# Kernel tuning notes

Measured on AMD Instinct MI355X. Metric: run time of the kernel, lower is better.

## Reference

```python
import jax, jax.numpy as jnp
import numpy as np

H = 8          # num_heads
KD = 64        # key_dim
R = 256        # num_random_features
EPS = 1e-3     # kernel_epsilon
SCALE = 1.0 / np.sqrt(KD)
CHUNK = 128    # chunk size for causal scan (math identical to full cumsum)


def setup_inputs() -> dict:
    key = jax.random.key(0)
    ks = jax.random.split(key, 7)
    B, S, D = 4, 4096, H * KD
    x = jax.random.normal(ks[0], (B, S, D), dtype=jnp.float32)
    Wq = jax.random.normal(ks[1], (D, D), dtype=jnp.float32) * 0.02
    Wk = jax.random.normal(ks[2], (D, D), dtype=jnp.float32) * 0.02
    Wv = jax.random.normal(ks[3], (D, D), dtype=jnp.float32) * 0.02
    Wo = jax.random.normal(ks[4], (D, D), dtype=jnp.float32) * 0.02
    bo = jnp.zeros((D,), dtype=jnp.float32)
    # random_features: orthogonal rows within each KD block (keras 'orthogonal' init approx)
    g = jax.random.normal(ks[5], (R, KD), dtype=jnp.float32)
    rf = jnp.concatenate([jnp.linalg.qr(b.T)[0].T for b in g.reshape(R // KD, KD, KD)], axis=0)
    return {"x": x, "Wq": Wq, "Wk": Wk, "Wv": Wv, "Wo": Wo, "bo": bo, "rf": rf}


def _kernel_features(z, rf):
    # z: [B,S,H,KD] -> [B,S,H,R]; scale applied AFTER projection as in source
    p = jnp.einsum('bshd,rd->bshr', z, rf) * SCALE
    p = p - jnp.max(p, axis=-1, keepdims=True)
    return jnp.exp(p) + EPS


def _causal_favor(qf, kf, v):
    # qf,kf: [B,S,H,R]; v: [B,S,H,KD]. Equivalent to cumsum of bshrd outer products.
    B, S, _, _ = qf.shape
    nc = S // CHUNK
    def to_chunks(t):
        return jnp.moveaxis(t.reshape(B, nc, CHUNK, *t.shape[2:]), 1, 0)
    qc_all, kc_all, vc_all = to_chunks(qf), to_chunks(kf), to_chunks(v)

    @jax.checkpoint
    def step(carry, inp):
        S0, Z0 = carry                     # S0: [B,H,R,KD], Z0: [B,H,R]
        qc, kc, vc = inp                   # [B,C,H,R], [B,C,H,R], [B,C,H,KD]
        kv = jnp.einsum('bchr,bchd->bchrd', kc, vc)
        kv_cum = jnp.cumsum(kv, axis=1) + S0[:, None]
        num = jnp.einsum('bchr,bchrd->bchd', qc, kv_cum)
        z_cum = jnp.cumsum(kc, axis=1) + Z0[:, None]
        den = jnp.einsum('bchr,bchr->bch', qc, z_cum) + EPS
        out = num / den[..., None]
        return (kv_cum[:, -1], z_cum[:, -1]), out

    S0 = jnp.zeros((B, H, R, KD), dtype=qf.dtype)
    Z0 = jnp.zeros((B, H, R), dtype=qf.dtype)
    _, outs = jax.lax.scan(step, (S0, Z0), (qc_all, kc_all, vc_all))
    return jnp.moveaxis(outs, 0, 1).reshape(B, S, H, KD)


def reference(x, Wq, Wk, Wv, Wo, bo, rf):
    B, S, D = x.shape
    q = (x @ Wq).reshape(B, S, H, KD)
    k = (x @ Wk).reshape(B, S, H, KD)
    v = (x @ Wv).reshape(B, S, H, KD)
    qf = _kernel_features(q, rf)
    kf = _kernel_features(k, rf)
    attn = _causal_favor(qf, kf, v)        # [B,S,H,KD]
    attn = attn.reshape(B, S, H * KD)
    return attn @ Wo + bo
```

## Files before the change

### kernel.cpp

```cpp
#include <hip/hip_runtime.h>
#include <stdint.h>


namespace {
constexpr int kB = 4;
constexpr int kS = 4096;
constexpr int kH = 8;
constexpr int kD = 512;
constexpr int kR = 256;
constexpr int kNC = 32;
constexpr float kEPS = 1e-3f;
constexpr float kSCALE = 0.125f;
constexpr int kSP = 80;
constexpr int kSST = kSP * 256;
}

typedef __attribute__((ext_vector_type(8))) short bf16x8;
typedef __attribute__((ext_vector_type(4))) float f32x4;

__device__ __forceinline__ f32x4 mfma16(bf16x8 a, bf16x8 b, f32x4 c) {
  return __builtin_amdgcn_mfma_f32_16x16x32_bf16(a, b, c, 0, 0, 0);
}

__device__ __forceinline__ float bflo(uint32_t w) {
  union { uint32_t u; float f; } c; c.u = w << 16; return c.f;
}
__device__ __forceinline__ float bfhi(uint32_t w) {
  union { uint32_t u; float f; } c; c.u = w & 0xffff0000u; return c.f;
}
__device__ __forceinline__ uint16_t f2bf(float x) {
  union { float f; uint32_t i; } c; c.f = x;
  uint32_t r = c.i + 0x7fffu + ((c.i >> 16) & 1u);
  return (uint16_t)(r >> 16);
}

__global__ __launch_bounds__(256) void cast_inputs(
    const float* __restrict__ x, const float* __restrict__ rfm,
    uint16_t* __restrict__ x16, uint16_t* __restrict__ rf16)
{
  int i4 = blockIdx.x * 256 + threadIdx.x;
  const int n1 = 2097152;
  const int n2 = 4096;
  const float* src; uint16_t* dst; int off;
  if (i4 < n1) { src = x; dst = x16; off = i4; }
  else if (i4 < n1 + n2) { src = rfm; dst = rf16; off = i4 - n1; }
  else return;
  float4 v = *(const float4*)(src + (size_t)off * 4);
  uint2 o;
  o.x = (uint32_t)f2bf(v.x) | ((uint32_t)f2bf(v.y) << 16);
  o.y = (uint32_t)f2bf(v.z) | ((uint32_t)f2bf(v.w) << 16);
  *(uint2*)(dst + (size_t)off * 4) = o;
}

__global__ __launch_bounds__(256) void transpose_w(
    const float* __restrict__ Wq, const float* __restrict__ Wk,
    const float* __restrict__ Wv, const float* __restrict__ Wo,
    uint16_t* __restrict__ WtBase)
{
  __shared__ uint16_t t16[64][72];
  const int z = blockIdx.z;
  const float* W = (z == 0) ? Wq : (z == 1) ? Wk : (z == 2) ? Wv : Wo;
  uint16_t* Wt = WtBase + (size_t)z * 262144;
  const int tid = threadIdx.x;
  const int k0 = blockIdx.x * 64, n0 = blockIdx.y * 64;
#pragma unroll
  for (int i = 0; i < 4; ++i) {
    int idx = tid + 256 * i;
    int kk = idx >> 4, nn4 = (idx & 15) * 4;
    float4 v = *(const float4*)(W + (size_t)(k0 + kk) * 512 + n0 + nn4);
    t16[kk][nn4 + 0] = f2bf(v.x);
    t16[kk][nn4 + 1] = f2bf(v.y);
    t16[kk][nn4 + 2] = f2bf(v.z);
    t16[kk][nn4 + 3] = f2bf(v.w);
  }
  __syncthreads();
#pragma unroll
  for (int i = 0; i < 4; ++i) {
    int idx = tid + 256 * i;
    int nn = idx >> 4, kk4 = (idx & 15) * 4;
    uint2 o;
    o.x = (uint32_t)t16[kk4 + 0][nn] | ((uint32_t)t16[kk4 + 1][nn] << 16);
    o.y = (uint32_t)t16[kk4 + 2][nn] | ((uint32_t)t16[kk4 + 3][nn] << 16);
    *(uint2*)(Wt + (size_t)(n0 + nn) * 512 + k0 + kk4) = o;
  }
}

template <bool BF16OUT>
__global__ __launch_bounds__(256) void gemm_bf16(
    const uint16_t* __restrict__ A, const uint16_t* __restrict__ Bt,
    const float* __restrict__ bias, void* __restrict__ O)
{
  const int tid = threadIdx.x;
  const int w = tid >> 6, lane = tid & 63;
  const int lr = lane & 15, lg = lane >> 4;
  const int m_base = blockIdx.x * 128 + w * 32;
  const int n_base = blockIdx.y * 64;

  f32x4 acc[2][4];
#pragma unroll
  for (int mf = 0; mf < 2; ++mf)
#pragma unroll
    for (int nf = 0; nf < 4; ++nf) acc[mf][nf] = (f32x4){0.f, 0.f, 0.f, 0.f};

  const uint16_t* a0p = A + (size_t)(m_base + lr) * 512 + 8 * lg;
  const uint16_t* a1p = a0p + (size_t)16 * 512;
  const uint16_t* bp = Bt + (size_t)(n_base + lr) * 512 + 8 * lg;

#pragma unroll
  for (int ks = 0; ks < 16; ++ks) {
    bf16x8 a0 = *(const bf16x8*)(a0p + ks * 32);
    bf16x8 a1 = *(const bf16x8*)(a1p + ks * 32);
#pragma unroll
    for (int nf = 0; nf < 4; ++nf) {
      bf16x8 b = *(const bf16x8*)(bp + (size_t)nf * 16 * 512 + ks * 32);
      acc[0][nf] = mfma16(a0, b, acc[0][nf]);
      acc[1][nf] = mfma16(a1, b, acc[1][nf]);
    }
  }

  float badd[4];
#pragma unroll
  for (int nf = 0; nf < 4; ++nf)
    badd[nf] = bias ? bias[n_base + nf * 16 + lr] : 0.0f;

  if constexpr (BF16OUT) {
    __shared__ uint16_t tr[4][32][72];
#pragma unroll
    for (int mf = 0; mf < 2; ++mf)
#pragma unroll
      for (int nf = 0; nf < 4; ++nf)
#pragma unroll
        for (int reg = 0; reg < 4; ++reg)
          tr[w][mf * 16 + 4 * lg + reg][nf * 16 + lr] = f2bf(acc[mf][nf][reg] + badd[nf]);
    __syncthreads();
#pragma unroll
    for (int it = 0; it < 4; ++it) {
      int idx = it * 64 + lane;
      int row = idx >> 3, c8 = (idx & 7) * 8;
      uint4 val = *(const uint4*)&tr[w][row][c8];
      *(uint4*)((uint16_t*)O + (size_t)(m_base + row) * 512 + n_base + c8) = val;
    }
  } else {
    __shared__ float trf[4][32][68];
#pragma unroll
    for (int mf = 0; mf < 2; ++mf)
#pragma unroll
      for (int nf = 0; nf < 4; ++nf)
#pragma unroll
        for (int reg = 0; reg < 4; ++reg)
          trf[w][mf * 16 + 4 * lg + reg][nf * 16 + lr] = acc[mf][nf][reg] + badd[nf];
    __syncthreads();
#pragma unroll
    for (int it = 0; it < 8; ++it) {
      int idx = it * 64 + lane;
      int row = idx >> 4, c4 = (idx & 15) * 4;
      float4 val = *(const float4*)&trf[w][row][c4];
      *(float4*)((float*)O + (size_t)(m_base + row) * 512 + n_base + c4) = val;
    }
  }
}

__global__ __launch_bounds__(256) void feat_mfma(
    const uint16_t* __restrict__ q16, const uint16_t* __restrict__ k16,
    const uint16_t* __restrict__ rf16,
    uint16_t* __restrict__ qf, uint16_t* __restrict__ kf)
{
  __shared__ uint16_t tr[4][16][264];
  const uint16_t* src = blockIdx.y ? k16 : q16;
  uint16_t* dst = blockIdx.y ? kf : qf;
  const int tgrp = blockIdx.x >> 3, h = blockIdx.x & 7;
  const int tid = threadIdx.x;
  const int w = tid >> 6, lane = tid & 63;
  const int lr = lane & 15, lg = lane >> 4;
  const int t0 = tgrp * 64 + w * 16;

  f32x4 acc[16];
#pragma unroll
  for (int nf = 0; nf < 16; ++nf) acc[nf] = (f32x4){0.f, 0.f, 0.f, 0.f};

  const uint16_t* ap = src + (size_t)(t0 + lr) * 512 + h * 64 + 8 * lg;
#pragma unroll
  for (int ks = 0; ks < 2; ++ks) {
    bf16x8 a = *(const bf16x8*)(ap + ks * 32);
#pragma unroll
    for (int nf = 0; nf < 16; ++nf) {
      bf16x8 b = *(const bf16x8*)(rf16 + (size_t)(nf * 16 + lr) * 64 + ks * 32 + 8 * lg);
      acc[nf] = mfma16(a, b, acc[nf]);
    }
  }

  float mx[4] = {-1e30f, -1e30f, -1e30f, -1e30f};
#pragma unroll
  for (int nf = 0; nf < 16; ++nf)
#pragma unroll
    for (int reg = 0; reg < 4; ++reg) {
      acc[nf][reg] *= kSCALE;
      mx[reg] = fmaxf(mx[reg], acc[nf][reg]);
    }
#pragma unroll
  for (int reg = 0; reg < 4; ++reg) {
    mx[reg] = fmaxf(mx[reg], __shfl_xor(mx[reg], 1));
    mx[reg] = fmaxf(mx[reg], __shfl_xor(mx[reg], 2));
    mx[reg] = fmaxf(mx[reg], __shfl_xor(mx[reg], 4));
    mx[reg] = fmaxf(mx[reg], __shfl_xor(mx[reg], 8));
  }
#pragma unroll
  for (int nf = 0; nf < 16; ++nf)
#pragma unroll
    for (int reg = 0; reg < 4; ++reg)
      tr[w][4 * lg + reg][nf * 16 + lr] = f2bf(__expf(acc[nf][reg] - mx[reg]) + kEPS);
  __syncthreads();
#pragma unroll
  for (int it = 0; it < 8; ++it) {
    int idx = it * 64 + lane;
    int row = idx >> 5, c8 = (idx & 31) * 8;
    uint4 val = *(const uint4*)&tr[w][row][c8];
    *(uint4*)(dst + ((size_t)(t0 + row) * 8 + h) * 256 + c8) = val;
  }
}

__global__ __launch_bounds__(256) void chunk_mfma(
    const uint16_t* __restrict__ kfeat, const uint16_t* __restrict__ vbuf,
    uint16_t* __restrict__ Skv)
{
  __shared__ uint16_t Vaug[80][136];
  __shared__ uint16_t uni2[21120];
  uint16_t (*kfT)[72] = (uint16_t (*)[72])uni2;
  uint16_t (*outT)[264] = (uint16_t (*)[264])uni2;

  const int c = blockIdx.x, bh = blockIdx.y;
  const int b = bh >> 3, h = bh & 7;
  const int tid = threadIdx.x;
  const int w = tid >> 6, lane = tid & 63;
  const int lr = lane & 15, lg = lane >> 4;
  const size_t srow = (size_t)b * kS + (size_t)c * 128;

#pragma unroll
  for (int i = 0; i < 4; ++i) {
    int idx = tid + 256 * i;
    int u = idx & 127, d = (idx >> 7) * 8;
    uint4 w8 = *(const uint4*)(vbuf + (srow + u) * kD + h * 64 + d);
    Vaug[d + 0][u] = (uint16_t)(w8.x & 0xffff);
    Vaug[d + 1][u] = (uint16_t)(w8.x >> 16);
    Vaug[d + 2][u] = (uint16_t)(w8.y & 0xffff);
    Vaug[d + 3][u] = (uint16_t)(w8.y >> 16);
    Vaug[d + 4][u] = (uint16_t)(w8.z & 0xffff);
    Vaug[d + 5][u] = (uint16_t)(w8.z >> 16);
    Vaug[d + 6][u] = (uint16_t)(w8.w & 0xffff);
    Vaug[d + 7][u] = (uint16_t)(w8.w >> 16);
  }
  if (tid < 128) Vaug[64][tid] = 0x3F80;
  if (tid < 136) {
#pragma unroll
    for (int rr = 65; rr < 80; ++rr) Vaug[rr][tid] = 0;
  }

  f32x4 acc[5][4];
#pragma unroll
  for (int mf = 0; mf < 5; ++mf)
#pragma unroll
    for (int nf = 0; nf < 4; ++nf) acc[mf][nf] = (f32x4){0.f, 0.f, 0.f, 0.f};

  const uint16_t* kp0 = kfeat + (srow * kH + h) * kR;
#pragma unroll
  for (int th = 0; th < 2; ++th) {
    if (th) __syncthreads();
    const uint16_t* kp = kp0 + (size_t)th * 64 * (kH * kR);
#pragma unroll
    for (int i = 0; i < 16; ++i) {
      int idx = tid + 256 * i;
      int t = idx >> 6, c4 = idx & 63;
      uint2 wv = *(const uint2*)(kp + (size_t)t * (kH * kR) + c4 * 4);
      int r = c4 * 4;
      kfT[r + 0][t] = (uint16_t)(wv.x & 0xffff);
      kfT[r + 1][t] = (uint16_t)(wv.x >> 16);
      kfT[r + 2][t] = (uint16_t)(wv.y & 0xffff);
      kfT[r + 3][t] = (uint16_t)(wv.y >> 16);
    }
    __syncthreads();
#pragma unroll
    for (int ks = 0; ks < 2; ++ks) {
      bf16x8 af[5];
#pragma unroll
      for (int mf = 0; mf < 5; ++mf)
        af[mf] = *(const bf16x8*)&Vaug[mf * 16 + lr][th * 64 + ks * 32 + 8 * lg];
#pragma unroll
      for (int nf = 0; nf < 4; ++nf) {
        bf16x8 kb = *(const bf16x8*)&kfT[w * 64 + nf * 16 + lr][ks * 32 + 8 * lg];
#pragma unroll
        for (int mf = 0; mf < 5; ++mf)
          acc[mf][nf] = mfma16(af[mf], kb, acc[mf][nf]);
      }
    }
  }

  __syncthreads();
#pragma unroll
  for (int mf = 0; mf < 5; ++mf)
#pragma unroll
    for (int nf = 0; nf < 4; ++nf)
#pragma unroll
      for (int reg = 0; reg < 4; ++reg)
        outT[mf * 16 + 4 * lg + reg][w * 64 + nf * 16 + lr] = f2bf(acc[mf][nf][reg]);
  __syncthreads();

  uint16_t* So = Skv + ((size_t)bh * kNC + c) * kSST;
#pragma unroll
  for (int it = 0; it < 10; ++it) {
    int idx = tid + 256 * it;
    int row = idx >> 5, c8 = (idx & 31) * 8;
    uint4 val = *(const uint4*)&outT[row][c8];
    *(uint4*)(So + (size_t)row * 256 + c8) = val;
  }
}

__global__ __launch_bounds__(256) void prefix_kernel(uint16_t* __restrict__ Skv)
{
  int e = blockIdx.x * 256 + threadIdx.x;
  int bh = e / kSST;
  int rd = e - bh * kSST;
  size_t base = (size_t)bh * kNC * kSST + rd;
  float run = 0.f;
  for (int c = 0; c < kNC; ++c) {
    size_t idx = base + (size_t)c * kSST;
    union { uint32_t i; float f; } cv; cv.i = ((uint32_t)Skv[idx]) << 16;
    Skv[idx] = f2bf(run);
    run += cv.f;
  }
}

__global__ __launch_bounds__(256) void favor_mfma(
    const uint16_t* __restrict__ qfeat, const uint16_t* __restrict__ kfeat,
    const uint16_t* __restrict__ vbuf, const uint16_t* __restrict__ Skv,
    uint16_t* __restrict__ attn16)
{
  __shared__ uint16_t Vaug[80][136];
  __shared__ uint16_t A_l[4][32][40];

  const int c = blockIdx.x, bh = blockIdx.y;
  const int b = bh >> 3, h = bh & 7;
  const int tid = threadIdx.x;
  const int w = tid >> 6, lane = tid & 63;
  const int lr = lane & 15, lg = lane >> 4;
  const size_t srow = (size_t)b * kS + (size_t)c * 128;

#pragma unroll
  for (int i = 0; i < 4; ++i) {
    int idx = tid + 256 * i;
    int u = idx & 127, d = (idx >> 7) * 8;
    uint4 w8 = *(const uint4*)(vbuf + (srow + u) * kD + h * 64 + d);
    Vaug[d + 0][u] = (uint16_t)(w8.x & 0xffff);
    Vaug[d + 1][u] = (uint16_t)(w8.x >> 16);
    Vaug[d + 2][u] = (uint16_t)(w8.y & 0xffff);
    Vaug[d + 3][u] = (uint16_t)(w8.y >> 16);
    Vaug[d + 4][u] = (uint16_t)(w8.z & 0xffff);
    Vaug[d + 5][u] = (uint16_t)(w8.z >> 16);
    Vaug[d + 6][u] = (uint16_t)(w8.w & 0xffff);
    Vaug[d + 7][u] = (uint16_t)(w8.w >> 16);
  }
  if (tid < 128) Vaug[64][tid] = 0x3F80;
  if (tid < 136) {
#pragma unroll
    for (int rr = 65; rr < 80; ++rr) Vaug[rr][tid] = 0;
  }

  bf16x8 qa[2][8];
  const uint16_t* qp = qfeat + ((srow + w * 32 + lr) * kH + h) * kR + 8 * lg;
#pragma unroll
  for (int mf = 0; mf < 2; ++mf)
#pragma unroll
    for (int ks = 0; ks < 8; ++ks)
      qa[mf][ks] = *(const bf16x8*)(qp + (size_t)mf * 16 * (kH * kR) + ks * 32);

  f32x4 o[2][5];
#pragma unroll
  for (int mf = 0; mf < 2; ++mf)
#pragma unroll
    for (int nf = 0; nf < 5; ++nf) o[mf][nf] = (f32x4){0.f, 0.f, 0.f, 0.f};

  const uint16_t* Sg = Skv + ((size_t)bh * kNC + c) * kSST + 8 * lg;
#pragma unroll
  for (int ks = 0; ks < 8; ++ks) {
#pragma unroll
    for (int nf = 0; nf < 5; ++nf) {
      bf16x8 sb = *(const bf16x8*)(Sg + (size_t)(nf * 16 + lr) * 256 + ks * 32);
      o[0][nf] = mfma16(qa[0][ks], sb, o[0][nf]);
      o[1][nf] = mfma16(qa[1][ks], sb, o[1][nf]);
    }
  }

  __syncthreads();

  const uint16_t* kp = kfeat + (srow + lr) * (kH * kR) + h * kR + 8 * lg;
  for (int ut = 0; ut <= w; ++ut) {
    f32x4 aacc[2][2];
#pragma unroll
    for (int mf = 0; mf < 2; ++mf)
#pragma unroll
      for (int nf = 0; nf < 2; ++nf) aacc[mf][nf] = (f32x4){0.f, 0.f, 0.f, 0.f};
#pragma unroll
    for (int ks = 0; ks < 8; ++ks) {
      bf16x8 kb0 = *(const bf16x8*)(kp + (size_t)(ut * 32) * (kH * kR) + ks * 32);
      bf16x8 kb1 = *(const bf16x8*)(kp + (size_t)(ut * 32 + 16) * (kH * kR) + ks * 32);
      aacc[0][0] = mfma16(qa[0][ks], kb0, aacc[0][0]);
      aacc[0][1] = mfma16(qa[0][ks], kb1, aacc[0][1]);
      aacc[1][0] = mfma16(qa[1][ks], kb0, aacc[1][0]);
      aacc[1][1] = mfma16(qa[1][ks], kb1, aacc[1][1]);
    }
#pragma unroll
    for (int mf = 0; mf < 2; ++mf)
#pragma unroll
      for (int nf = 0; nf < 2; ++nf)
#pragma unroll
        for (int reg = 0; reg < 4; ++reg) {
          int trow = mf * 16 + 4 * lg + reg;
          int ucol = nf * 16 + lr;
          float v = aacc[mf][nf][reg];
          if (ut == w && ucol > trow) v = 0.0f;
          A_l[w][trow][ucol] = f2bf(v);
        }
    bf16x8 af0 = *(const bf16x8*)&A_l[w][lr][8 * lg];
    bf16x8 af1 = *(const bf16x8*)&A_l[w][16 + lr][8 * lg];
#pragma unroll
    for (int nf = 0; nf < 5; ++nf) {
      bf16x8 vb = *(const bf16x8*)&Vaug[nf * 16 + lr][ut * 32 + 8 * lg];
      o[0][nf] = mfma16(af0, vb, o[0][nf]);
      o[1][nf] = mfma16(af1, vb, o[1][nf]);
    }
  }

#pragma unroll
  for (int mf = 0; mf < 2; ++mf) {
    float inv[4];
#pragma unroll
    for (int reg = 0; reg < 4; ++reg) {
      float den = __shfl(o[mf][4][reg], lane & 48);
      inv[reg] = 1.0f / (den + kEPS);
    }
    const size_t trow = srow + w * 32 + mf * 16 + 4 * lg;
#pragma unroll
    for (int reg = 0; reg < 4; ++reg) {
      uint16_t* op = attn16 + (trow + reg) * kD + h * 64 + lr;
#pragma unroll
      for (int nf = 0; nf < 4; ++nf)
        op[nf * 16] = f2bf(o[mf][nf][reg] * inv[reg]);
    }
  }
}

extern "C" void kernel_launch(void* const* d_in, const int* in_sizes, int n_in,
                              void* d_out, int out_size, void* d_ws, size_t ws_size,
                              hipStream_t stream)
{
  (void)in_sizes; (void)n_in; (void)out_size; (void)ws_size;
  const float* x  = (const float*)d_in[0];
  const float* Wq = (const float*)d_in[1];
  const float* Wk = (const float*)d_in[2];
  const float* Wv = (const float*)d_in[3];
  const float* Wo = (const float*)d_in[4];
  const float* bo = (const float*)d_in[5];
  const float* rf = (const float*)d_in[6];
  float* out = (float*)d_out;

  char* ws = (char*)d_ws;
  uint16_t* x16   = (uint16_t*)ws;
  uint16_t* k16   = (uint16_t*)(ws + (16u << 20));
  uint16_t* v16   = (uint16_t*)(ws + (32u << 20));
  uint16_t* qf    = (uint16_t*)(ws + (48u << 20));
  uint16_t* kf    = (uint16_t*)(ws + (112u << 20));
  uint16_t* Skv   = (uint16_t*)(ws + (176u << 20));
  uint16_t* Wt    = (uint16_t*)(ws + (216u << 20));
  uint16_t* rf16  = Wt + 4 * 262144;
  uint16_t* q16   = (uint16_t*)d_out;
  uint16_t* attn16 = k16;

  cast_inputs<<<dim3(8208, 1, 1), 256, 0, stream>>>(x, rf, x16, rf16);
  transpose_w<<<dim3(8, 8, 4), 256, 0, stream>>>(Wq, Wk, Wv, Wo, Wt);

  gemm_bf16<true><<<dim3(128, 8, 1), 256, 0, stream>>>(x16, Wt + 0 * 262144, nullptr, q16);
  gemm_bf16<true><<<dim3(128, 8, 1), 256, 0, stream>>>(x16, Wt + 1 * 262144, nullptr, k16);
  gemm_bf16<true><<<dim3(128, 8, 1), 256, 0, stream>>>(x16, Wt + 2 * 262144, nullptr, v16);

  feat_mfma<<<dim3(2048, 2, 1), 256, 0, stream>>>(q16, k16, rf16, qf, kf);

  chunk_mfma<<<dim3(kNC, kB * kH, 1), 256, 0, stream>>>(kf, v16, Skv);
  prefix_kernel<<<dim3(2560, 1, 1), 256, 0, stream>>>(Skv);
  favor_mfma<<<dim3(kNC, kB * kH, 1), 256, 0, stream>>>(qf, kf, v16, Skv, attn16);

  gemm_bf16<false><<<dim3(128, 8, 1), 256, 0, stream>>>(attn16, Wt + 3 * 262144, bo, out);
}
```

Baseline: 397.2 us.

## Fold random-feature projection into Wq/Wk and fuse QK projection with feature map

```diff
diff --git a/kernel.cpp b/kernel.cpp
--- a/kernel.cpp
+++ b/kernel.cpp
@@ -36,15 +36,19 @@
 
 __global__ __launch_bounds__(256) void cast_inputs(
     const float* __restrict__ x, const float* __restrict__ rfm,
-    uint16_t* __restrict__ x16, uint16_t* __restrict__ rf16)
+    const float* __restrict__ Wq, const float* __restrict__ Wk,
+    uint16_t* __restrict__ x16, uint16_t* __restrict__ rf16,
+    uint16_t* __restrict__ Wq16, uint16_t* __restrict__ Wk16)
 {
   int i4 = blockIdx.x * 256 + threadIdx.x;
   const int n1 = 2097152;
   const int n2 = 4096;
+  const int n3 = 65536;
   const float* src; uint16_t* dst; int off;
   if (i4 < n1) { src = x; dst = x16; off = i4; }
   else if (i4 < n1 + n2) { src = rfm; dst = rf16; off = i4 - n1; }
-  else return;
+  else if (i4 < n1 + n2 + n3) { src = Wq; dst = Wq16; off = i4 - n1 - n2; }
+  else { src = Wk; dst = Wk16; off = i4 - n1 - n2 - n3; }
   float4 v = *(const float4*)(src + (size_t)off * 4);
   uint2 o;
   o.x = (uint32_t)f2bf(v.x) | ((uint32_t)f2bf(v.y) << 16);
@@ -53,13 +57,12 @@
 }
 
 __global__ __launch_bounds__(256) void transpose_w(
-    const float* __restrict__ Wq, const float* __restrict__ Wk,
     const float* __restrict__ Wv, const float* __restrict__ Wo,
     uint16_t* __restrict__ WtBase)
 {
   __shared__ uint16_t t16[64][72];
   const int z = blockIdx.z;
-  const float* W = (z == 0) ? Wq : (z == 1) ? Wk : (z == 2) ? Wv : Wo;
+  const float* W = z ? Wo : Wv;
   uint16_t* Wt = WtBase + (size_t)z * 262144;
   const int tid = threadIdx.x;
   const int k0 = blockIdx.x * 64, n0 = blockIdx.y * 64;
@@ -85,6 +88,49 @@
   }
 }
 
+__global__ __launch_bounds__(256) void make_wrf(
+    const uint16_t* __restrict__ Wq16, const uint16_t* __restrict__ Wk16,
+    const uint16_t* __restrict__ rf16, uint16_t* __restrict__ WrfBase)
+{
+  __shared__ uint16_t tr[4][16][136];
+  const uint16_t* W16 = blockIdx.z ? Wk16 : Wq16;
+  uint16_t* out = WrfBase + (size_t)blockIdx.z * 1048576;
+  const int h = blockIdx.y;
+  const int tid = threadIdx.x;
+  const int w = tid >> 6, lane = tid & 63;
+  const int lr = lane & 15, lg = lane >> 4;
+  const int r0 = blockIdx.x * 64 + w * 16;
+
+  bf16x8 a0 = *(const bf16x8*)(rf16 + (size_t)(r0 + lr) * 64 + 8 * lg);
+  bf16x8 a1 = *(const bf16x8*)(rf16 + (size_t)(r0 + lr) * 64 + 32 + 8 * lg);
+
+  for (int kb = 0; kb < 4; ++kb) {
+    f32x4 acc[8];
+#pragma unroll
+    for (int nf = 0; nf < 8; ++nf) acc[nf] = (f32x4){0.f, 0.f, 0.f, 0.f};
+#pragma unroll
+    for (int nf = 0; nf < 8; ++nf) {
+      int kcol = kb * 128 + nf * 16 + lr;
+      bf16x8 b0 = *(const bf16x8*)(W16 + (size_t)kcol * 512 + h * 64 + 8 * lg);
+      bf16x8 b1 = *(const bf16x8*)(W16 + (size_t)kcol * 512 + h * 64 + 32 + 8 * lg);
+      acc[nf] = mfma16(a0, b0, acc[nf]);
+      acc[nf] = mfma16(a1, b1, acc[nf]);
+    }
+#pragma unroll
+    for (int nf = 0; nf < 8; ++nf)
+#pragma unroll
+      for (int reg = 0; reg < 4; ++reg)
+        tr[w][4 * lg + reg][nf * 16 + lr] = f2bf(acc[nf][reg]);
+#pragma unroll
+    for (int it = 0; it < 4; ++it) {
+      int idx = it * 64 + lane;
+      int row = idx >> 4, c8 = (idx & 15) * 8;
+      uint4 val = *(const uint4*)&tr[w][row][c8];
+      *(uint4*)(out + (size_t)(h * 256 + r0 + row) * 512 + kb * 128 + c8) = val;
+    }
+  }
+}
+
 template <bool BF16OUT>
 __global__ __launch_bounds__(256) void gemm_bf16(
     const uint16_t* __restrict__ A, const uint16_t* __restrict__ Bt,
@@ -160,62 +206,83 @@
   }
 }
 
-__global__ __launch_bounds__(256) void feat_mfma(
-    const uint16_t* __restrict__ q16, const uint16_t* __restrict__ k16,
-    const uint16_t* __restrict__ rf16,
+__global__ __launch_bounds__(256) void qkf_gemm(
+    const uint16_t* __restrict__ x16, const uint16_t* __restrict__ WrfBase,
     uint16_t* __restrict__ qf, uint16_t* __restrict__ kf)
 {
+  __shared__ uint16_t Bs[256 * 32];
   __shared__ uint16_t tr[4][16][264];
-  const uint16_t* src = blockIdx.y ? k16 : q16;
-  uint16_t* dst = blockIdx.y ? kf : qf;
-  const int tgrp = blockIdx.x >> 3, h = blockIdx.x & 7;
+  const uint16_t* Bt = WrfBase + (size_t)blockIdx.z * 1048576 +
+                       (size_t)blockIdx.y * 256 * 512;
+  uint16_t* dst = blockIdx.z ? kf : qf;
+  const int h = blockIdx.y;
   const int tid = threadIdx.x;
   const int w = tid >> 6, lane = tid & 63;
   const int lr = lane & 15, lg = lane >> 4;
-  const int t0 = tgrp * 64 + w * 16;
-
-  f32x4 acc[16];
-#pragma unroll
-  for (int nf = 0; nf < 16; ++nf) acc[nf] = (f32x4){0.f, 0.f, 0.f, 0.f};
-
-  const uint16_t* ap = src + (size_t)(t0 + lr) * 512 + h * 64 + 8 * lg;
-#pragma unroll
-  for (int ks = 0; ks < 2; ++ks) {
-    bf16x8 a = *(const bf16x8*)(ap + ks * 32);
+  const int m_base = blockIdx.x * 128 + w * 32;
+
+  f32x4 acc[2][16];
+#pragma unroll
+  for (int mf = 0; mf < 2; ++mf)
+#pragma unroll
+    for (int nf = 0; nf < 16; ++nf) acc[mf][nf] = (f32x4){0.f, 0.f, 0.f, 0.f};
+
+  const uint16_t* a0p = x16 + (size_t)(m_base + lr) * 512 + 8 * lg;
+
+  for (int ks = 0; ks < 16; ++ks) {
+    __syncthreads();
+#pragma unroll
+    for (int i = 0; i < 4; ++i) {
+      int idx = tid + 256 * i;
+      int row = idx >> 2, j = idx & 3;
+      uint4 v = *(const uint4*)(Bt + (size_t)row * 512 + ks * 32 + j * 8);
+      int byteoff = row * 64 + ((j * 16) ^ (((row >> 1) & 3) << 4));
+      *(uint4*)((char*)Bs + byteoff) = v;
+    }
+    __syncthreads();
+    bf16x8 a0 = *(const bf16x8*)(a0p + ks * 32);
+    bf16x8 a1 = *(const bf16x8*)(a0p + 16 * 512 + ks * 32);
 #pragma unroll
     for (int nf = 0; nf < 16; ++nf) {
-      bf16x8 b = *(const bf16x8*)(rf16 + (size_t)(nf * 16 + lr) * 64 + ks * 32 + 8 * lg);
-      acc[nf] = mfma16(a, b, acc[nf]);
-    }
-  }
-
-  float mx[4] = {-1e30f, -1e30f, -1e30f, -1e30f};
-#pragma unroll
-  for (int nf = 0; nf < 16; ++nf)
+      int row = nf * 16 + lr;
+      int byteoff = row * 64 + ((lg * 16) ^ (((row >> 1) & 3) << 4));
+      bf16x8 b = *(const bf16x8*)((char*)Bs + byteoff);
+      acc[0][nf] = mfma16(a0, b, acc[0][nf]);
+      acc[1][nf] = mfma16(a1, b, acc[1][nf]);
+    }
+  }
+
+#pragma unroll
+  for (int mf = 0; mf < 2; ++mf) {
+    float mx[4] = {-1e30f, -1e30f, -1e30f, -1e30f};
+#pragma unroll
+    for (int nf = 0; nf < 16; ++nf)
+#pragma unroll
+      for (int reg = 0; reg < 4; ++reg) {
+        acc[mf][nf][reg] *= kSCALE;
+        mx[reg] = fmaxf(mx[reg], acc[mf][nf][reg]);
+      }
 #pragma unroll
     for (int reg = 0; reg < 4; ++reg) {
-      acc[nf][reg] *= kSCALE;
-      mx[reg] = fmaxf(mx[reg], acc[nf][reg]);
-    }
-#pragma unroll
-  for (int reg = 0; reg < 4; ++reg) {
-    mx[reg] = fmaxf(mx[reg], __shfl_xor(mx[reg], 1));
-    mx[reg] = fmaxf(mx[reg], __shfl_xor(mx[reg], 2));
-    mx[reg] = fmaxf(mx[reg], __shfl_xor(mx[reg], 4));
-    mx[reg] = fmaxf(mx[reg], __shfl_xor(mx[reg], 8));
-  }
-#pragma unroll
-  for (int nf = 0; nf < 16; ++nf)
-#pragma unroll
-    for (int reg = 0; reg < 4; ++reg)
-      tr[w][4 * lg + reg][nf * 16 + lr] = f2bf(__expf(acc[nf][reg] - mx[reg]) + kEPS);
-  __syncthreads();
-#pragma unroll
-  for (int it = 0; it < 8; ++it) {
-    int idx = it * 64 + lane;
-    int row = idx >> 5, c8 = (idx & 31) * 8;
-    uint4 val = *(const uint4*)&tr[w][row][c8];
-    *(uint4*)(dst + ((size_t)(t0 + row) * 8 + h) * 256 + c8) = val;
+      mx[reg] = fmaxf(mx[reg], __shfl_xor(mx[reg], 1));
+      mx[reg] = fmaxf(mx[reg], __shfl_xor(mx[reg], 2));
+      mx[reg] = fmaxf(mx[reg], __shfl_xor(mx[reg], 4));
+      mx[reg] = fmaxf(mx[reg], __shfl_xor(mx[reg], 8));
+    }
+#pragma unroll
+    for (int nf = 0; nf < 16; ++nf)
+#pragma unroll
+      for (int reg = 0; reg < 4; ++reg)
+        tr[w][4 * lg + reg][nf * 16 + lr] =
+            f2bf(__expf(acc[mf][nf][reg] - mx[reg]) + kEPS);
+#pragma unroll
+    for (int it = 0; it < 8; ++it) {
+      int idx = it * 64 + lane;
+      int row = idx >> 5, c8 = (idx & 31) * 8;
+      uint4 val = *(const uint4*)&tr[w][row][c8];
+      size_t t = (size_t)m_base + mf * 16 + row;
+      *(uint4*)(dst + (t * 8 + h) * 256 + c8) = val;
+    }
   }
 }
 
@@ -462,30 +529,31 @@
   const float* rf = (const float*)d_in[6];
   float* out = (float*)d_out;
 
+  const size_t MiB = 1048576;
   char* ws = (char*)d_ws;
-  uint16_t* x16   = (uint16_t*)ws;
-  uint16_t* k16   = (uint16_t*)(ws + (16u << 20));
-  uint16_t* v16   = (uint16_t*)(ws + (32u << 20));
-  uint16_t* qf    = (uint16_t*)(ws + (48u << 20));
-  uint16_t* kf    = (uint16_t*)(ws + (112u << 20));
-  uint16_t* Skv   = (uint16_t*)(ws + (176u << 20));
-  uint16_t* Wt    = (uint16_t*)(ws + (216u << 20));
-  uint16_t* rf16  = Wt + 4 * 262144;
-  uint16_t* q16   = (uint16_t*)d_out;
-  uint16_t* attn16 = k16;
-
-  cast_inputs<<<dim3(8208, 1, 1), 256, 0, stream>>>(x, rf, x16, rf16);
-  transpose_w<<<dim3(8, 8, 4), 256, 0, stream>>>(Wq, Wk, Wv, Wo, Wt);
-
-  gemm_bf16<true><<<dim3(128, 8, 1), 256, 0, stream>>>(x16, Wt + 0 * 262144, nullptr, q16);
-  gemm_bf16<true><<<dim3(128, 8, 1), 256, 0, stream>>>(x16, Wt + 1 * 262144, nullptr, k16);
-  gemm_bf16<true><<<dim3(128, 8, 1), 256, 0, stream>>>(x16, Wt + 2 * 262144, nullptr, v16);
-
-  feat_mfma<<<dim3(2048, 2, 1), 256, 0, stream>>>(q16, k16, rf16, qf, kf);
+  uint16_t* x16    = (uint16_t*)ws;
+  uint16_t* attn16 = (uint16_t*)(ws + 16 * MiB);
+  uint16_t* v16    = (uint16_t*)(ws + 32 * MiB);
+  uint16_t* qf     = (uint16_t*)(ws + 48 * MiB);
+  uint16_t* kf     = (uint16_t*)(ws + 112 * MiB);
+  uint16_t* Skv    = (uint16_t*)(ws + 176 * MiB);
+  uint16_t* Wt     = (uint16_t*)(ws + 216 * MiB);
+  uint16_t* Wrf    = (uint16_t*)(ws + 217 * MiB);
+  uint16_t* Wq16   = (uint16_t*)(ws + 221 * MiB);
+  uint16_t* Wk16   = Wq16 + 262144;
+  uint16_t* rf16   = (uint16_t*)(ws + 222 * MiB);
+
+  cast_inputs<<<dim3(8720, 1, 1), 256, 0, stream>>>(x, rf, Wq, Wk,
+                                                    x16, rf16, Wq16, Wk16);
+  transpose_w<<<dim3(8, 8, 2), 256, 0, stream>>>(Wv, Wo, Wt);
+  make_wrf<<<dim3(4, 8, 2), 256, 0, stream>>>(Wq16, Wk16, rf16, Wrf);
+
+  gemm_bf16<true><<<dim3(128, 8, 1), 256, 0, stream>>>(x16, Wt, nullptr, v16);
+  qkf_gemm<<<dim3(128, 8, 2), 256, 0, stream>>>(x16, Wrf, qf, kf);
 
   chunk_mfma<<<dim3(kNC, kB * kH, 1), 256, 0, stream>>>(kf, v16, Skv);
   prefix_kernel<<<dim3(2560, 1, 1), 256, 0, stream>>>(Skv);
   favor_mfma<<<dim3(kNC, kB * kH, 1), 256, 0, stream>>>(qf, kf, v16, Skv, attn16);
 
-  gemm_bf16<false><<<dim3(128, 8, 1), 256, 0, stream>>>(attn16, Wt + 3 * 262144, bo, out);
-}
+  gemm_bf16<false><<<dim3(128, 8, 1), 256, 0, stream>>>(attn16, Wt + 262144, bo, out);
+}
```

Result: slower. 443.6 us (+11.7%).

## Fuse Q/K projection GEMMs with random-feature kernel computation

Applied to the files above, without the earlier changes.

```diff
diff --git a/kernel.cpp b/kernel.cpp
--- a/kernel.cpp
+++ b/kernel.cpp
@@ -10,7 +10,6 @@
 constexpr int kR = 256;
 constexpr int kNC = 32;
 constexpr float kEPS = 1e-3f;
-constexpr float kSCALE = 0.125f;
 constexpr int kSP = 80;
 constexpr int kSST = kSP * 256;
 }
@@ -22,12 +21,6 @@
   return __builtin_amdgcn_mfma_f32_16x16x32_bf16(a, b, c, 0, 0, 0);
 }
 
-__device__ __forceinline__ float bflo(uint32_t w) {
-  union { uint32_t u; float f; } c; c.u = w << 16; return c.f;
-}
-__device__ __forceinline__ float bfhi(uint32_t w) {
-  union { uint32_t u; float f; } c; c.u = w & 0xffff0000u; return c.f;
-}
 __device__ __forceinline__ uint16_t f2bf(float x) {
   union { float f; uint32_t i; } c; c.f = x;
   uint32_t r = c.i + 0x7fffu + ((c.i >> 16) & 1u);
@@ -160,62 +153,116 @@
   }
 }
 
-__global__ __launch_bounds__(256) void feat_mfma(
-    const uint16_t* __restrict__ q16, const uint16_t* __restrict__ k16,
+__global__ __launch_bounds__(256) void gemm_feat(
+    const uint16_t* __restrict__ x16, const uint16_t* __restrict__ WtBase,
     const uint16_t* __restrict__ rf16,
     uint16_t* __restrict__ qf, uint16_t* __restrict__ kf)
 {
-  __shared__ uint16_t tr[4][16][264];
-  const uint16_t* src = blockIdx.y ? k16 : q16;
-  uint16_t* dst = blockIdx.y ? kf : qf;
-  const int tgrp = blockIdx.x >> 3, h = blockIdx.x & 7;
+  __shared__ uint16_t rf_l[256][72];
+  __shared__ uint16_t trbuf[4][2176];
+
+  const uint16_t* Bt = WtBase + (size_t)blockIdx.z * 262144;
+  uint16_t* dst = blockIdx.z ? kf : qf;
+  const int h = blockIdx.y;
   const int tid = threadIdx.x;
   const int w = tid >> 6, lane = tid & 63;
   const int lr = lane & 15, lg = lane >> 4;
-  const int t0 = tgrp * 64 + w * 16;
-
-  f32x4 acc[16];
-#pragma unroll
-  for (int nf = 0; nf < 16; ++nf) acc[nf] = (f32x4){0.f, 0.f, 0.f, 0.f};
-
-  const uint16_t* ap = src + (size_t)(t0 + lr) * 512 + h * 64 + 8 * lg;
+  const int m_base = blockIdx.x * 128 + w * 32;
+
+#pragma unroll
+  for (int i = 0; i < 8; ++i) {
+    int idx = tid + 256 * i;
+    int row = idx >> 3, c8 = (idx & 7) * 8;
+    uint4 v = *(const uint4*)(rf16 + (size_t)row * 64 + c8);
+    *(uint4*)&rf_l[row][c8] = v;
+  }
+  __syncthreads();
+
+  f32x4 acc[2][4];
+#pragma unroll
+  for (int mf = 0; mf < 2; ++mf)
+#pragma unroll
+    for (int nf = 0; nf < 4; ++nf) acc[mf][nf] = (f32x4){0.f, 0.f, 0.f, 0.f};
+
+  const uint16_t* a0p = x16 + (size_t)(m_base + lr) * 512 + 8 * lg;
+  const uint16_t* a1p = a0p + (size_t)16 * 512;
+  const uint16_t* bp = Bt + (size_t)(h * 64 + lr) * 512 + 8 * lg;
+
+#pragma unroll
+  for (int ks = 0; ks < 16; ++ks) {
+    bf16x8 a0 = *(const bf16x8*)(a0p + ks * 32);
+    bf16x8 a1 = *(const bf16x8*)(a1p + ks * 32);
+#pragma unroll
+    for (int nf = 0; nf < 4; ++nf) {
+      bf16x8 b = *(const bf16x8*)(bp + (size_t)nf * 16 * 512 + ks * 32);
+      acc[0][nf] = mfma16(a0, b, acc[0][nf]);
+      acc[1][nf] = mfma16(a1, b, acc[1][nf]);
+    }
+  }
+
+  uint16_t (*trw)[72] = (uint16_t (*)[72])&trbuf[w][0];
+  bf16x8 qa[2][2];
+#pragma unroll
+  for (int mf = 0; mf < 2; ++mf) {
+#pragma unroll
+    for (int nf = 0; nf < 4; ++nf)
+#pragma unroll
+      for (int reg = 0; reg < 4; ++reg)
+        trw[4 * lg + reg][nf * 16 + lr] = f2bf(acc[mf][nf][reg] * 0.125f);
+    qa[mf][0] = *(const bf16x8*)&trw[lr][8 * lg];
+    qa[mf][1] = *(const bf16x8*)&trw[lr][32 + 8 * lg];
+  }
+
+  f32x4 acc2[2][16];
+#pragma unroll
+  for (int mf = 0; mf < 2; ++mf)
+#pragma unroll
+    for (int nf = 0; nf < 16; ++nf) acc2[mf][nf] = (f32x4){0.f, 0.f, 0.f, 0.f};
 #pragma unroll
   for (int ks = 0; ks < 2; ++ks) {
-    bf16x8 a = *(const bf16x8*)(ap + ks * 32);
 #pragma unroll
     for (int nf = 0; nf < 16; ++nf) {
-      bf16x8 b = *(const bf16x8*)(rf16 + (size_t)(nf * 16 + lr) * 64 + ks * 32 + 8 * lg);
-      acc[nf] = mfma16(a, b, acc[nf]);
-    }
-  }
-
-  float mx[4] = {-1e30f, -1e30f, -1e30f, -1e30f};
-#pragma unroll
-  for (int nf = 0; nf < 16; ++nf)
+      bf16x8 b = *(const bf16x8*)&rf_l[nf * 16 + lr][ks * 32 + 8 * lg];
+      acc2[0][nf] = mfma16(qa[0][ks], b, acc2[0][nf]);
+      acc2[1][nf] = mfma16(qa[1][ks], b, acc2[1][nf]);
+    }
+  }
+
+  uint16_t (*trh)[136] = (uint16_t (*)[136])&trbuf[w][0];
+#pragma unroll
+  for (int mf = 0; mf < 2; ++mf) {
+    float mx[4] = {-1e30f, -1e30f, -1e30f, -1e30f};
+#pragma unroll
+    for (int nf = 0; nf < 16; ++nf)
+#pragma unroll
+      for (int reg = 0; reg < 4; ++reg)
+        mx[reg] = fmaxf(mx[reg], acc2[mf][nf][reg]);
 #pragma unroll
     for (int reg = 0; reg < 4; ++reg) {
-      acc[nf][reg] *= kSCALE;
-      mx[reg] = fmaxf(mx[reg], acc[nf][reg]);
-    }
-#pragma unroll
-  for (int reg = 0; reg < 4; ++reg) {
-    mx[reg] = fmaxf(mx[reg], __shfl_xor(mx[reg], 1));
-    mx[reg] = fmaxf(mx[reg], __shfl_xor(mx[reg], 2));
-    mx[reg] = fmaxf(mx[reg], __shfl_xor(mx[reg], 4));
-    mx[reg] = fmaxf(mx[reg], __shfl_xor(mx[reg], 8));
-  }
-#pragma unroll
-  for (int nf = 0; nf < 16; ++nf)
-#pragma unroll
-    for (int reg = 0; reg < 4; ++reg)
-      tr[w][4 * lg + reg][nf * 16 + lr] = f2bf(__expf(acc[nf][reg] - mx[reg]) + kEPS);
-  __syncthreads();
-#pragma unroll
-  for (int it = 0; it < 8; ++it) {
-    int idx = it * 64 + lane;
-    int row = idx >> 5, c8 = (idx & 31) * 8;
-    uint4 val = *(const uint4*)&tr[w][row][c8];
-    *(uint4*)(dst + ((size_t)(t0 + row) * 8 + h) * 256 + c8) = val;
+      mx[reg] = fmaxf(mx[reg], __shfl_xor(mx[reg], 1));
+      mx[reg] = fmaxf(mx[reg], __shfl_xor(mx[reg], 2));
+      mx[reg] = fmaxf(mx[reg], __shfl_xor(mx[reg], 4));
+      mx[reg] = fmaxf(mx[reg], __shfl_xor(mx[reg], 8));
+    }
+#pragma unroll
+    for (int half = 0; half < 2; ++half) {
+#pragma unroll
+      for (int nf8 = 0; nf8 < 8; ++nf8) {
+        int nf = half * 8 + nf8;
+#pragma unroll
+        for (int reg = 0; reg < 4; ++reg)
+          trh[4 * lg + reg][nf8 * 16 + lr] =
+              f2bf(__expf(acc2[mf][nf][reg] - mx[reg]) + kEPS);
+      }
+#pragma unroll
+      for (int it = 0; it < 4; ++it) {
+        int idx = it * 64 + lane;
+        int row = idx >> 4, c8 = (idx & 15) * 8;
+        uint4 val = *(const uint4*)&trh[row][c8];
+        size_t t = (size_t)m_base + mf * 16 + row;
+        *(uint4*)(dst + (t * 8 + h) * 256 + half * 128 + c8) = val;
+      }
+    }
   }
 }
 
@@ -462,26 +509,23 @@
   const float* rf = (const float*)d_in[6];
   float* out = (float*)d_out;
 
+  const size_t MiB = 1048576;
   char* ws = (char*)d_ws;
-  uint16_t* x16   = (uint16_t*)ws;
-  uint16_t* k16   = (uint16_t*)(ws + (16u << 20));
-  uint16_t* v16   = (uint16_t*)(ws + (32u << 20));
-  uint16_t* qf    = (uint16_t*)(ws + (48u << 20));
-  uint16_t* kf    = (uint16_t*)(ws + (112u << 20));
-  uint16_t* Skv   = (uint16_t*)(ws + (176u << 20));
-  uint16_t* Wt    = (uint16_t*)(ws + (216u << 20));
-  uint16_t* rf16  = Wt + 4 * 262144;
-  uint16_t* q16   = (uint16_t*)d_out;
-  uint16_t* attn16 = k16;
+  uint16_t* x16    = (uint16_t*)ws;
+  uint16_t* attn16 = (uint16_t*)(ws + 16 * MiB);
+  uint16_t* v16    = (uint16_t*)(ws + 32 * MiB);
+  uint16_t* qf     = (uint16_t*)(ws + 48 * MiB);
+  uint16_t* kf     = (uint16_t*)(ws + 112 * MiB);
+  uint16_t* Skv    = (uint16_t*)(ws + 176 * MiB);
+  uint16_t* Wt     = (uint16_t*)(ws + 216 * MiB);
+  uint16_t* rf16   = (uint16_t*)(ws + 218 * MiB);
 
   cast_inputs<<<dim3(8208, 1, 1), 256, 0, stream>>>(x, rf, x16, rf16);
   transpose_w<<<dim3(8, 8, 4), 256, 0, stream>>>(Wq, Wk, Wv, Wo, Wt);
 
-  gemm_bf16<true><<<dim3(128, 8, 1), 256, 0, stream>>>(x16, Wt + 0 * 262144, nullptr, q16);
-  gemm_bf16<true><<<dim3(128, 8, 1), 256, 0, stream>>>(x16, Wt + 1 * 262144, nullptr, k16);
+  gemm_feat<<<dim3(128, 8, 2), 256, 0, stream>>>(x16, Wt, rf16, qf, kf);
+
   gemm_bf16<true><<<dim3(128, 8, 1), 256, 0, stream>>>(x16, Wt + 2 * 262144, nullptr, v16);
-
-  feat_mfma<<<dim3(2048, 2, 1), 256, 0, stream>>>(q16, k16, rf16, qf, kf);
 
   chunk_mfma<<<dim3(kNC, kB * kH, 1), 256, 0, stream>>>(kf, v16, Skv);
   prefix_kernel<<<dim3(2560, 1, 1), 256, 0, stream>>>(Skv);
```

Result: faster. 326.8 us (-17.7%).
